# Kernel tuning notes

Measured on AMD Instinct MI355X. Metric: run time of the kernel, lower is better.

Reference implementation:

```python
import jax, jax.numpy as jnp
import numpy as np

# Hard-coded constants from the original module
GAMMA = 0.1      # self.gamma default
N_STEPS = 10     # self.n_steps default
RHO = 0.9        # RMSProp decay
LR = 0.009       # RMSProp learning rate
MOM = 0.9        # momentum
EPS = 1e-8       # RMSProp epsilon
ABS_EPS = 1e-6   # diff_abs smoothing: diff_abs(x) = sqrt(x^2 + 1e-6)

B, IN_DIM, OUT_DIM = 4096, 2048, 4096


def setup_inputs() -> dict:
    key = jax.random.key(0)
    k1, k2 = jax.random.split(key)
    inputs = jax.random.normal(k1, (B, IN_DIM), dtype=jnp.float32)
    # keras 'uniform' init: U(-0.05, 0.05), shape (output_dim, input_dim)
    W = jax.random.uniform(k2, (OUT_DIM, IN_DIM), minval=-0.05, maxval=0.05, dtype=jnp.float32)
    return {"inputs": inputs, "W": W}


def reference(inputs, W):
    batch = inputs.shape[0]
    out_dim = W.shape[0]
    a = jnp.sqrt(inputs * inputs + ABS_EPS)          # diff_abs(inputs), [B, in_dim]
    act = lambda u: 0.5 * (1.0 + jnp.exp(-u))        # self.activation

    def cost(x):
        # l1_norm.sum() + l1_inov + own_norm  (prior = 0)
        l1 = (GAMMA * act(x @ W) * a).sum()
        l1_inov = (GAMMA / 10.0) * jnp.sum(x * x)
        own = GAMMA * jnp.sum(jnp.sqrt(x * x + ABS_EPS))
        return l1 + l1_inov + own

    grad_cost = jax.grad(cost)

    def step(carry, _):
        x, acc1, acc2 = carry
        g = grad_cost(x)                              # [B, out_dim]
        new_acc1 = RHO * acc1 + (1.0 - RHO) * g * g
        denom = jnp.sqrt(new_acc1 + EPS)
        new_acc2 = MOM * acc2 - LR * g / denom
        cand = x - LR * g / denom
        t = 0.1 * LR / denom                          # elementwise prox threshold
        new_x = jnp.maximum(cand - t, 0.0) + jnp.minimum(cand + t, 0.0) + MOM * new_acc2
        new_x = jax.lax.stop_gradient(new_x)          # theano disconnected_grad
        return (new_x, new_acc1, new_acc2), None

    z = jnp.zeros((batch, out_dim), dtype=inputs.dtype)
    # scan runs n_steps; last step's l1_norm uses the state after n_steps-1 updates,
    # so run n_steps-1 updates then compute the final l1_norm directly.
    (x, _, _), _ = jax.lax.scan(step, (z, z, z), None, length=N_STEPS - 1)
    return GAMMA * act(x @ W) * a                     # outputs[-1][-1]: last l1_norm, [B, in_dim]
```

## Files before the change

### kernel.cpp

```cpp
#include <hip/hip_runtime.h>
#include <cstdint>
#include <cstddef>

#define B_DIM   4096
#define IN_DIM  2048
#define OUT_DIM 4096

typedef __attribute__((ext_vector_type(8))) __bf16 bf16x8;
typedef __attribute__((ext_vector_type(4))) float  f32x4;
typedef unsigned short ushortT;

__device__ __forceinline__ ushortT f2bf(float f) {
    unsigned int u = __float_as_uint(f);
    u += 0x7FFFu + ((u >> 16) & 1u);
    return (ushortT)(u >> 16);
}
__device__ __forceinline__ float bf2f(ushortT b) {
    return __uint_as_float(((unsigned int)b) << 16);
}

__device__ __forceinline__ void gload16(const void* g, void* l) {
    __builtin_amdgcn_global_load_lds(
        (const __attribute__((address_space(1))) void*)g,
        (__attribute__((address_space(3))) void*)l, 16, 0, 0);
}

__global__ void prep_g0_kernel(const float* __restrict__ in, ushortT* __restrict__ Gb,
                               ushortT* __restrict__ negA) {
    int i = blockIdx.x * 256 + threadIdx.x;
    float4 v = reinterpret_cast<const float4*>(in)[i];
    ushort4 g;
    g.x = f2bf(-0.05f * sqrtf(v.x * v.x + 1e-6f));
    g.y = f2bf(-0.05f * sqrtf(v.y * v.y + 1e-6f));
    g.z = f2bf(-0.05f * sqrtf(v.z * v.z + 1e-6f));
    g.w = f2bf(-0.05f * sqrtf(v.w * v.w + 1e-6f));
    reinterpret_cast<ushort4*>(Gb)[i]   = g;
    reinterpret_cast<ushort4*>(negA)[i] = g;
}

__global__ void conv_w_kernel(const float* __restrict__ W, ushortT* __restrict__ Wb,
                              ushortT* __restrict__ WTb) {
    __shared__ float tile[64][65];
    const int i0 = blockIdx.x * 64;
    const int j0 = blockIdx.y * 64;
    const int c  = threadIdx.x & 63;
    const int rq = threadIdx.x >> 6;
#pragma unroll
    for (int rp = 0; rp < 16; ++rp) {
        int row = rp * 4 + rq;
        float w = W[(size_t)(j0 + row) * IN_DIM + i0 + c];
        tile[row][c] = w;
        Wb[(size_t)(j0 + row) * IN_DIM + i0 + c] = f2bf(w);
    }
    __syncthreads();
#pragma unroll
    for (int rp = 0; rp < 16; ++rp) {
        int row = rp * 4 + rq;
        WTb[(size_t)(i0 + row) * OUT_DIM + j0 + c] = f2bf(tile[c][row]);
    }
}

#define EPILOGUE(MR_)                                                          \
    float* lep = (float*)(smem + w * 4352);                                    \
    const int li = lane >> 4;                                                  \
    const int lc = lane & 15;                                                  \
    _Pragma("unroll")                                                          \
    for (int m = 0; m < (MR_); ++m) {                                          \
        _Pragma("unroll")                                                      \
        for (int n = 0; n < 4; ++n)                                            \
            _Pragma("unroll")                                                  \
            for (int i = 0; i < 4; ++i)                                        \
                lep[(li * 4 + i) * 68 + n * 16 + lc] = acc[m][n][i];           \
        asm volatile("s_waitcnt lgkmcnt(0)" ::: "memory");                     \
        __builtin_amdgcn_sched_barrier(0);                                     \
        _Pragma("unroll")                                                      \
        for (int rr = 0; rr < 4; ++rr) {                                       \
            const int row = rr + li * 4;                                       \
            float4 v = *reinterpret_cast<const float4*>(&lep[row * 68 + lc * 4]); \
            const size_t idx  = (size_t)(row0w + m * 16 + row) * N + col0w + lc * 4; \
            const size_t idx4 = idx >> 2;                                      \
            if constexpr (EPI == 0) {                                          \
                ushort4 au = *reinterpret_cast<const ushort4*>(&nega[idx]);    \
                ushort4 g;                                                     \
                g.x = f2bf(bf2f(au.x) * expf(-v.x));                           \
                g.y = f2bf(bf2f(au.y) * expf(-v.y));                           \
                g.z = f2bf(bf2f(au.z) * expf(-v.z));                           \
                g.w = f2bf(bf2f(au.w) * expf(-v.w));                           \
                *reinterpret_cast<ushort4*>(&Gb[idx]) = g;                     \
            } else if constexpr (EPI == 1) {                                   \
                float4 iv = reinterpret_cast<const float4*>(inb)[idx4];        \
                float4 o;                                                      \
                o.x = 0.05f * (1.0f + expf(-v.x)) * sqrtf(iv.x * iv.x + 1e-6f); \
                o.y = 0.05f * (1.0f + expf(-v.y)) * sqrtf(iv.y * iv.y + 1e-6f); \
                o.z = 0.05f * (1.0f + expf(-v.z)) * sqrtf(iv.z * iv.z + 1e-6f); \
                o.w = 0.05f * (1.0f + expf(-v.w)) * sqrtf(iv.w * iv.w + 1e-6f); \
                reinterpret_cast<float4*>(out)[idx4] = o;                      \
            } else {                                                           \
                ushort4 xu  = *reinterpret_cast<const ushort4*>(&xb[idx]);     \
                ushort4 a1u = *reinterpret_cast<const ushort4*>(&acc1[idx]);   \
                ushort4 a2u = *reinterpret_cast<const ushort4*>(&acc2[idx]);   \
                float xs[4] = {bf2f(xu.x), bf2f(xu.y), bf2f(xu.z), bf2f(xu.w)}; \
                float vs[4] = {v.x, v.y, v.z, v.w};                            \
                ushortT a1s[4] = {a1u.x, a1u.y, a1u.z, a1u.w};                 \
                ushortT a2s[4] = {a2u.x, a2u.y, a2u.z, a2u.w};                 \
                ushortT a1n[4], a2n[4], xbn[4];                                \
                _Pragma("unroll")                                              \
                for (int j = 0; j < 4; ++j) {                                  \
                    float g    = vs[j] + 0.02f * xs[j] + 0.1f * xs[j] * rsqrtf(xs[j] * xs[j] + 1e-6f); \
                    float a1   = 0.9f * bf2f(a1s[j]) + 0.1f * g * g;           \
                    float inv  = rsqrtf(a1 + 1e-8f);                           \
                    float r_   = 0.009f * g * inv;                             \
                    float a2   = 0.9f * bf2f(a2s[j]) - r_;                     \
                    float cand = xs[j] - r_;                                   \
                    float t_   = 0.0009f * inv;                                \
                    float xn   = fmaxf(cand - t_, 0.0f) + fminf(cand + t_, 0.0f) + 0.9f * a2; \
                    a1n[j] = f2bf(a1); a2n[j] = f2bf(a2); xbn[j] = f2bf(xn);   \
                }                                                              \
                *reinterpret_cast<ushort4*>(&acc1[idx]) = make_ushort4(a1n[0], a1n[1], a1n[2], a1n[3]); \
                *reinterpret_cast<ushort4*>(&acc2[idx]) = make_ushort4(a2n[0], a2n[1], a2n[2], a2n[3]); \
                *reinterpret_cast<ushort4*>(&xb[idx])   = make_ushort4(xbn[0], xbn[1], xbn[2], xbn[3]); \
            }                                                                  \
        }                                                                      \
        asm volatile("s_waitcnt lgkmcnt(0)" ::: "memory");                     \
    }

#define PHASE(MB, RB, SLOTP, STTILE, C0, NC)                                   \
    {                                                                          \
        const char* sb_ = (SLOTP);                                             \
        if (RB) {                                                              \
            _Pragma("unroll")                                                  \
            for (int n = 0; n < 4; ++n)                                        \
                bF[n] = *reinterpret_cast<const bf16x8*>(sb_ + bRd[n]);        \
        }                                                                      \
        bf16x8 aF[4];                                                          \
        _Pragma("unroll")                                                      \
        for (int m = 0; m < 4; ++m)                                            \
            aF[m] = *reinterpret_cast<const bf16x8*>(sb_ + aRd[m]);            \
        if ((STTILE) < nt) {                                                   \
            _Pragma("unroll")                                                  \
            for (int c = 0; c < (NC); ++c) stage_chunk((STTILE), (C0) + c);    \
        }                                                                      \
        __builtin_amdgcn_sched_barrier(0);                                     \
        __builtin_amdgcn_s_barrier();                                          \
        asm volatile("s_waitcnt lgkmcnt(0)" ::: "memory");                     \
        __builtin_amdgcn_sched_barrier(0);                                     \
        __builtin_amdgcn_s_setprio(1);                                         \
        _Pragma("unroll")                                                      \
        for (int m = 0; m < 4; ++m) {                                          \
            _Pragma("unroll")                                                  \
            for (int n = 0; n < 4; ++n)                                        \
                acc[m][n] = __builtin_amdgcn_mfma_f32_16x16x32_bf16(           \
                    aF[m], bF[n], acc[m][n], 0, 0, 0);                         \
        }                                                                      \
        __builtin_amdgcn_s_setprio(0);                                         \
        __builtin_amdgcn_s_barrier();                                          \
        __builtin_amdgcn_sched_barrier(0);                                     \
    }

template <int EPI>
__global__ __launch_bounds__(512, 1)
void gemm_phase(const ushortT* __restrict__ A, const ushortT* __restrict__ Bm,
                int N, int K,
                const float* __restrict__ inb, const ushortT* __restrict__ nega,
                ushortT* __restrict__ Gb, float* __restrict__ out,
                ushortT* __restrict__ acc1, ushortT* __restrict__ acc2,
                ushortT* __restrict__ xb) {
    constexpr int BM = 128, BN = 256;
    constexpr int ASZ  = BM * 64;
    constexpr int SLOT = ASZ + BN * 64;
    constexpr int LA   = 1, LB = 2, L = 3;
    __shared__ alignas(16) char smem[4 * SLOT];

    const int tid  = threadIdx.x;
    const int lane = tid & 63;
    const int w    = tid >> 6;
    const int wm   = w >> 2;
    const int wn   = w & 3;
    const int nbx  = N / BN;
    const int nwg  = gridDim.x;
    const int cpx  = nwg >> 3;
    const int bid  = (int)blockIdx.x;
    const int swz  = (bid & 7) * cpx + (bid >> 3);
    const int bx   = swz % nbx;
    const int by   = swz / nbx;
    const int row0 = by * BM;
    const int col0 = bx * BN;
    const size_t strideK2 = (size_t)K * 2;

    const char* gp[L]; int lo[L];
#pragma unroll
    for (int i = 0; i < LA; ++i) {
        int Lp  = i * 512 + tid;
        int row = Lp >> 2, sl = Lp & 3;
        int src = sl ^ ((row >> 1) & 3);
        gp[i] = (const char*)A + (size_t)(row0 + row) * strideK2 + src * 16;
        lo[i] = i * 8192 + w * 1024;
    }
#pragma unroll
    for (int i = 0; i < LB; ++i) {
        int Lp  = i * 512 + tid;
        int row = Lp >> 2, sl = Lp & 3;
        int src = sl ^ ((row >> 1) & 3);
        gp[LA + i] = (const char*)Bm + (size_t)(col0 + row) * strideK2 + src * 16;
        lo[LA + i] = ASZ + i * 8192 + w * 1024;
    }
    auto stage_all = [&](int tt) {
        char* sb = smem + (tt & 3) * SLOT;
        const size_t kb = (size_t)tt * 64;
#pragma unroll
        for (int c = 0; c < L; ++c) gload16(gp[c] + kb, sb + lo[c]);
    };
    auto stage_chunk = [&](int tt, int c) {
        gload16(gp[c] + (size_t)tt * 64, smem + (tt & 3) * SLOT + lo[c]);
    };

    int aRd[4], bRd[4];
#pragma unroll
    for (int m = 0; m < 4; ++m) {
        int row = wm * 64 + m * 16 + (lane & 15);
        aRd[m] = row * 64 + (((lane >> 4) ^ ((row >> 1) & 3)) * 16);
    }
#pragma unroll
    for (int n = 0; n < 4; ++n) {
        int row = wn * 64 + n * 16 + (lane & 15);
        bRd[n] = ASZ + row * 64 + (((lane >> 4) ^ ((row >> 1) & 3)) * 16);
    }

    f32x4 acc[4][4] = {};
    const int nt = K >> 5;

    stage_all(0); stage_all(1); stage_all(2);

    for (int tt = 0; tt < nt; tt += 2) {
        if (tt + 2 < nt) asm volatile("s_waitcnt vmcnt(%0)" :: "n"(L) : "memory");
        else             asm volatile("s_waitcnt vmcnt(0)"  ::: "memory");
        __builtin_amdgcn_s_barrier();
        __builtin_amdgcn_sched_barrier(0);

        const char* sb0 = smem + (tt & 3) * SLOT;
        const char* sb1 = smem + ((tt + 1) & 3) * SLOT;
        bf16x8 bF[4];
        PHASE(0, true, sb0, tt + 3, 0, 3)
        PHASE(0, true, sb1, tt + 4, 0, 3)
    }

    __builtin_amdgcn_s_barrier();
    const int row0w = row0 + wm * 64;
    const int col0w = col0 + wn * 64;
    EPILOGUE(4)
}

template <int EPI>
__global__ __launch_bounds__(512, 4)
void gemm_mb(const ushortT* __restrict__ A, const ushortT* __restrict__ Bm,
             int N, int K,
             const float* __restrict__ inb, const ushortT* __restrict__ nega,
             ushortT* __restrict__ Gb, float* __restrict__ out,
             ushortT* __restrict__ acc1, ushortT* __restrict__ acc2,
             ushortT* __restrict__ xb) {
    constexpr int BM = 256, BN = 128;
    constexpr int ASZ  = BM * 64;
    constexpr int SLOT = ASZ + BN * 64;
    constexpr int CA   = 2, CB = 1, L = 3;
    __shared__ alignas(16) char smem[3 * SLOT];

    const int tid  = threadIdx.x;
    const int lane = tid & 63;
    const int w    = tid >> 6;
    const int wm   = w >> 1;
    const int wn   = w & 1;
    const int nbx  = N / BN;
    const int nwg  = gridDim.x;
    const int cpx  = nwg >> 3;
    const int bid  = (int)blockIdx.x;
    const int swz  = (bid & 7) * cpx + (bid >> 3);
    const int bx   = swz % nbx;
    const int by   = swz / nbx;
    const int row0 = by * BM;
    const int col0 = bx * BN;
    const size_t strideK2 = (size_t)K * 2;

    const char* gp[L]; int lo[L];
#pragma unroll
    for (int c = 0; c < CA; ++c) {
        int Lp  = c * 512 + tid;
        int row = Lp >> 2, sl = Lp & 3;
        int src = sl ^ ((row >> 1) & 3);
        gp[c] = (const char*)A + (size_t)(row0 + row) * strideK2 + src * 16;
        lo[c] = c * 8192 + w * 1024;
    }
#pragma unroll
    for (int c = 0; c < CB; ++c) {
        int Lp  = c * 512 + tid;
        int row = Lp >> 2, sl = Lp & 3;
        int src = sl ^ ((row >> 1) & 3);
        gp[CA + c] = (const char*)Bm + (size_t)(col0 + row) * strideK2 + src * 16;
        lo[CA + c] = ASZ + c * 8192 + w * 1024;
    }
    auto stage = [&](int tt) {
        char* sb = smem + (tt % 3) * SLOT;
        const size_t kb = (size_t)tt * 64;
#pragma unroll
        for (int c = 0; c < L; ++c) gload16(gp[c] + kb, sb + lo[c]);
    };

    int aRd[4], bRd[4];
#pragma unroll
    for (int m = 0; m < 4; ++m) {
        int row = wm * 64 + m * 16 + (lane & 15);
        aRd[m] = row * 64 + (((lane >> 4) ^ ((row >> 1) & 3)) * 16);
    }
#pragma unroll
    for (int n = 0; n < 4; ++n) {
        int row = wn * 64 + n * 16 + (lane & 15);
        bRd[n] = ASZ + row * 64 + (((lane >> 4) ^ ((row >> 1) & 3)) * 16);
    }

    f32x4 acc[4][4] = {};
    const int nt = K >> 5;

    stage(0); stage(1);

    for (int tt = 0; tt < nt; ++tt) {
        if (tt < nt - 1) asm volatile("s_waitcnt vmcnt(%0)" :: "n"(L) : "memory");
        else             asm volatile("s_waitcnt vmcnt(0)"  ::: "memory");
        __builtin_amdgcn_s_barrier();
        __builtin_amdgcn_sched_barrier(0);

        const char* sb = smem + (tt % 3) * SLOT;
        bf16x8 aF[4], bF[4];
#pragma unroll
        for (int n = 0; n < 4; ++n) bF[n] = *reinterpret_cast<const bf16x8*>(sb + bRd[n]);
#pragma unroll
        for (int m = 0; m < 4; ++m) aF[m] = *reinterpret_cast<const bf16x8*>(sb + aRd[m]);
        if (tt + 2 < nt) stage(tt + 2);
        __builtin_amdgcn_s_setprio(1);
#pragma unroll
        for (int m = 0; m < 4; ++m)
#pragma unroll
            for (int n = 0; n < 4; ++n)
                acc[m][n] = __builtin_amdgcn_mfma_f32_16x16x32_bf16(aF[m], bF[n], acc[m][n], 0, 0, 0);
        __builtin_amdgcn_s_setprio(0);
    }

    __builtin_amdgcn_s_barrier();
    const int row0w = row0 + wm * 64;
    const int col0w = col0 + wn * 64;
    EPILOGUE(4)
}

extern "C" void kernel_launch(void* const* d_in, const int* in_sizes, int n_in,
                              void* d_out, int out_size, void* d_ws, size_t ws_size,
                              hipStream_t stream) {
    const float* in = (const float*)d_in[0];
    const float* W  = (const float*)d_in[1];
    float* out = (float*)d_out;
    char* ws = (char*)d_ws;

    ushortT* acc1 = (ushortT*)(ws);
    ushortT* acc2 = (ushortT*)(ws + ((size_t)32  << 20));
    ushortT* xb   = (ushortT*)(ws + ((size_t)64  << 20));
    ushortT* Wb   = (ushortT*)(ws + ((size_t)96  << 20));
    ushortT* WTb  = (ushortT*)(ws + ((size_t)112 << 20));
    ushortT* Gb   = (ushortT*)(ws + ((size_t)128 << 20));
    ushortT* negA = (ushortT*)(ws + ((size_t)144 << 20));

    hipMemsetAsync(ws, 0, (size_t)96 << 20, stream);

    prep_g0_kernel<<<dim3(B_DIM * IN_DIM / 4 / 256), dim3(256), 0, stream>>>(in, Gb, negA);
    conv_w_kernel<<<dim3(IN_DIM / 64, OUT_DIM / 64), dim3(256), 0, stream>>>(W, Wb, WTb);

    for (int step = 0; step < 9; ++step) {
        if (step > 0) {
            gemm_phase<0><<<dim3(256), dim3(512), 0, stream>>>(
                xb, WTb, IN_DIM, OUT_DIM, nullptr, negA, Gb, nullptr, nullptr, nullptr, nullptr);
        }
        gemm_mb<2><<<dim3(512), dim3(512), 0, stream>>>(
            Gb, Wb, OUT_DIM, IN_DIM, nullptr, nullptr, nullptr, nullptr, acc1, acc2, xb);
    }
    gemm_phase<1><<<dim3(256), dim3(512), 0, stream>>>(
        xb, WTb, IN_DIM, OUT_DIM, in, nullptr, nullptr, out, nullptr, nullptr, nullptr);
}
```

Measured before the change: 1.563 ms.

## Retile the update GEMM to 256 threads and specialize the zero-state first step

The update GEMM now runs 4 waves per block, each computing a 128x64 sub-tile instead of 64x64, to raise MFMA-to-LDS-read reuse, at the cost of more registers and fewer waves. The first step uses a specialized epilogue that assumes zero initial x/acc1/acc2, so the 96MB workspace memset and the state reads are removed. The gradient epilogue also switches to the fast __expf intrinsic, which trades some accuracy for cheaper exponentials.

```diff
diff --git a/kernel.cpp b/kernel.cpp
--- a/kernel.cpp
+++ b/kernel.cpp
@@ -82,10 +82,10 @@
             if constexpr (EPI == 0) {                                          \
                 ushort4 au = *reinterpret_cast<const ushort4*>(&nega[idx]);    \
                 ushort4 g;                                                     \
-                g.x = f2bf(bf2f(au.x) * expf(-v.x));                           \
-                g.y = f2bf(bf2f(au.y) * expf(-v.y));                           \
-                g.z = f2bf(bf2f(au.z) * expf(-v.z));                           \
-                g.w = f2bf(bf2f(au.w) * expf(-v.w));                           \
+                g.x = f2bf(bf2f(au.x) * __expf(-v.x));                         \
+                g.y = f2bf(bf2f(au.y) * __expf(-v.y));                         \
+                g.z = f2bf(bf2f(au.z) * __expf(-v.z));                         \
+                g.w = f2bf(bf2f(au.w) * __expf(-v.w));                         \
                 *reinterpret_cast<ushort4*>(&Gb[idx]) = g;                     \
             } else if constexpr (EPI == 1) {                                   \
                 float4 iv = reinterpret_cast<const float4*>(inb)[idx4];        \
@@ -95,6 +95,24 @@
                 o.z = 0.05f * (1.0f + expf(-v.z)) * sqrtf(iv.z * iv.z + 1e-6f); \
                 o.w = 0.05f * (1.0f + expf(-v.w)) * sqrtf(iv.w * iv.w + 1e-6f); \
                 reinterpret_cast<float4*>(out)[idx4] = o;                      \
+            } else if constexpr (EPI == 3) {                                   \
+                float vs[4] = {v.x, v.y, v.z, v.w};                            \
+                ushortT a1n[4], a2n[4], xbn[4];                                \
+                _Pragma("unroll")                                              \
+                for (int j = 0; j < 4; ++j) {                                  \
+                    float g    = vs[j];                                        \
+                    float a1   = 0.1f * g * g;                                 \
+                    float inv  = rsqrtf(a1 + 1e-8f);                           \
+                    float r_   = 0.009f * g * inv;                             \
+                    float a2   = -r_;                                          \
+                    float cand = -r_;                                          \
+                    float t_   = 0.0009f * inv;                                \
+                    float xn   = fmaxf(cand - t_, 0.0f) + fminf(cand + t_, 0.0f) + 0.9f * a2; \
+                    a1n[j] = f2bf(a1); a2n[j] = f2bf(a2); xbn[j] = f2bf(xn);   \
+                }                                                              \
+                *reinterpret_cast<ushort4*>(&acc1[idx]) = make_ushort4(a1n[0], a1n[1], a1n[2], a1n[3]); \
+                *reinterpret_cast<ushort4*>(&acc2[idx]) = make_ushort4(a2n[0], a2n[1], a2n[2], a2n[3]); \
+                *reinterpret_cast<ushort4*>(&xb[idx])   = make_ushort4(xbn[0], xbn[1], xbn[2], xbn[3]); \
             } else {                                                           \
                 ushort4 xu  = *reinterpret_cast<const ushort4*>(&xb[idx]);     \
                 ushort4 a1u = *reinterpret_cast<const ushort4*>(&acc1[idx]);   \
@@ -251,17 +269,17 @@
 }
 
 template <int EPI>
-__global__ __launch_bounds__(512, 4)
-void gemm_mb(const ushortT* __restrict__ A, const ushortT* __restrict__ Bm,
-             int N, int K,
-             const float* __restrict__ inb, const ushortT* __restrict__ nega,
-             ushortT* __restrict__ Gb, float* __restrict__ out,
-             ushortT* __restrict__ acc1, ushortT* __restrict__ acc2,
-             ushortT* __restrict__ xb) {
+__global__ __launch_bounds__(256, 2)
+void gemm_mb4(const ushortT* __restrict__ A, const ushortT* __restrict__ Bm,
+              int N, int K,
+              const float* __restrict__ inb, const ushortT* __restrict__ nega,
+              ushortT* __restrict__ Gb, float* __restrict__ out,
+              ushortT* __restrict__ acc1, ushortT* __restrict__ acc2,
+              ushortT* __restrict__ xb) {
     constexpr int BM = 256, BN = 128;
     constexpr int ASZ  = BM * 64;
     constexpr int SLOT = ASZ + BN * 64;
-    constexpr int CA   = 2, CB = 1, L = 3;
+    constexpr int CA   = 4, CB = 2, L = 6;
     __shared__ alignas(16) char smem[3 * SLOT];
 
     const int tid  = threadIdx.x;
@@ -283,19 +301,19 @@
     const char* gp[L]; int lo[L];
 #pragma unroll
     for (int c = 0; c < CA; ++c) {
-        int Lp  = c * 512 + tid;
+        int Lp  = c * 256 + tid;
         int row = Lp >> 2, sl = Lp & 3;
         int src = sl ^ ((row >> 1) & 3);
         gp[c] = (const char*)A + (size_t)(row0 + row) * strideK2 + src * 16;
-        lo[c] = c * 8192 + w * 1024;
+        lo[c] = c * 4096 + w * 1024;
     }
 #pragma unroll
     for (int c = 0; c < CB; ++c) {
-        int Lp  = c * 512 + tid;
+        int Lp  = c * 256 + tid;
         int row = Lp >> 2, sl = Lp & 3;
         int src = sl ^ ((row >> 1) & 3);
         gp[CA + c] = (const char*)Bm + (size_t)(col0 + row) * strideK2 + src * 16;
-        lo[CA + c] = ASZ + c * 8192 + w * 1024;
+        lo[CA + c] = ASZ + c * 4096 + w * 1024;
     }
     auto stage = [&](int tt) {
         char* sb = smem + (tt % 3) * SLOT;
@@ -304,10 +322,10 @@
         for (int c = 0; c < L; ++c) gload16(gp[c] + kb, sb + lo[c]);
     };
 
-    int aRd[4], bRd[4];
-#pragma unroll
-    for (int m = 0; m < 4; ++m) {
-        int row = wm * 64 + m * 16 + (lane & 15);
+    int aRd[8], bRd[4];
+#pragma unroll
+    for (int m = 0; m < 8; ++m) {
+        int row = wm * 128 + m * 16 + (lane & 15);
         aRd[m] = row * 64 + (((lane >> 4) ^ ((row >> 1) & 3)) * 16);
     }
 #pragma unroll
@@ -316,7 +334,7 @@
         bRd[n] = ASZ + row * 64 + (((lane >> 4) ^ ((row >> 1) & 3)) * 16);
     }
 
-    f32x4 acc[4][4] = {};
+    f32x4 acc[8][4] = {};
     const int nt = K >> 5;
 
     stage(0); stage(1);
@@ -328,15 +346,15 @@
         __builtin_amdgcn_sched_barrier(0);
 
         const char* sb = smem + (tt % 3) * SLOT;
-        bf16x8 aF[4], bF[4];
+        bf16x8 aF[8], bF[4];
 #pragma unroll
         for (int n = 0; n < 4; ++n) bF[n] = *reinterpret_cast<const bf16x8*>(sb + bRd[n]);
 #pragma unroll
-        for (int m = 0; m < 4; ++m) aF[m] = *reinterpret_cast<const bf16x8*>(sb + aRd[m]);
+        for (int m = 0; m < 8; ++m) aF[m] = *reinterpret_cast<const bf16x8*>(sb + aRd[m]);
         if (tt + 2 < nt) stage(tt + 2);
         __builtin_amdgcn_s_setprio(1);
 #pragma unroll
-        for (int m = 0; m < 4; ++m)
+        for (int m = 0; m < 8; ++m)
 #pragma unroll
             for (int n = 0; n < 4; ++n)
                 acc[m][n] = __builtin_amdgcn_mfma_f32_16x16x32_bf16(aF[m], bF[n], acc[m][n], 0, 0, 0);
@@ -344,9 +362,9 @@
     }
 
     __builtin_amdgcn_s_barrier();
-    const int row0w = row0 + wm * 64;
+    const int row0w = row0 + wm * 128;
     const int col0w = col0 + wn * 64;
-    EPILOGUE(4)
+    EPILOGUE(8)
 }
 
 extern "C" void kernel_launch(void* const* d_in, const int* in_sizes, int n_in,
@@ -365,17 +383,16 @@
     ushortT* Gb   = (ushortT*)(ws + ((size_t)128 << 20));
     ushortT* negA = (ushortT*)(ws + ((size_t)144 << 20));
 
-    hipMemsetAsync(ws, 0, (size_t)96 << 20, stream);
 
     prep_g0_kernel<<<dim3(B_DIM * IN_DIM / 4 / 256), dim3(256), 0, stream>>>(in, Gb, negA);
     conv_w_kernel<<<dim3(IN_DIM / 64, OUT_DIM / 64), dim3(256), 0, stream>>>(W, Wb, WTb);
 
-    for (int step = 0; step < 9; ++step) {
-        if (step > 0) {
-            gemm_phase<0><<<dim3(256), dim3(512), 0, stream>>>(
-                xb, WTb, IN_DIM, OUT_DIM, nullptr, negA, Gb, nullptr, nullptr, nullptr, nullptr);
-        }
-        gemm_mb<2><<<dim3(512), dim3(512), 0, stream>>>(
+    gemm_mb4<3><<<dim3(512), dim3(256), 0, stream>>>(
+        Gb, Wb, OUT_DIM, IN_DIM, nullptr, nullptr, nullptr, nullptr, acc1, acc2, xb);
+    for (int step = 1; step < 9; ++step) {
+        gemm_phase<0><<<dim3(256), dim3(512), 0, stream>>>(
+            xb, WTb, IN_DIM, OUT_DIM, nullptr, negA, Gb, nullptr, nullptr, nullptr, nullptr);
+        gemm_mb4<2><<<dim3(512), dim3(256), 0, stream>>>(
             Gb, Wb, OUT_DIM, IN_DIM, nullptr, nullptr, nullptr, nullptr, acc1, acc2, xb);
     }
     gemm_phase<1><<<dim3(256), dim3(512), 0, stream>>>(
```

Result: no change. 1.536 ms (-1.7%).
